# Performance work log

Hardware: AMD Instinct MI355X
Metric: run time of the kernel (lower is better)

## Reference

```python
import jax, jax.numpy as jnp
import numpy as np

DELTA_V = 0.5
DELTA_D = 3.0
ALPHA = 1.0
BETA = 1.0
GAMMA = 0.001
K = 5  # max instance label (labels 1..K; 0 = background)


def setup_inputs() -> dict:
    key = jax.random.key(0)
    k1, k2 = jax.random.split(key)
    B, D, H, W = 8, 8, 512, 1024
    embedding = jax.random.normal(k1, (B, D, H, W), dtype=jnp.float32)
    instance_mask = jax.random.randint(k2, (B, H, W), 0, K + 1, dtype=jnp.int32)
    return {"embedding": embedding, "instance_mask": instance_mask}


def _disc_loss(embedding, instance_mask):
    B, D, H, W = embedding.shape
    P = H * W
    emb = embedding.transpose(0, 2, 3, 1).reshape(B, P, D)      # [B,P,D]
    labels = instance_mask.reshape(B, P)                         # [B,P]

    # one-hot over instance labels 1..K (background excluded)
    onehot = (labels[..., None] == jnp.arange(1, K + 1, dtype=labels.dtype)).astype(emb.dtype)  # [B,P,K]
    counts = onehot.sum(axis=1)                                  # [B,K]
    present = counts > 0                                         # [B,K]
    presentf = present.astype(emb.dtype)
    N = presentf.sum(axis=-1)                                    # [B] num instances

    # per-instance centers via segment mean
    sums = jnp.einsum('bpd,bpk->bkd', emb, onehot)               # [B,K,D]
    centers = sums / jnp.maximum(counts, 1.0)[..., None]         # [B,K,D]

    # ---- variance loss: per-pixel distance to own center ----
    idx = jnp.clip(labels - 1, 0, K - 1)                         # [B,P]
    c_pix = jnp.take_along_axis(centers, idx[..., None], axis=1) # [B,P,D]
    d = jnp.sqrt(jnp.sum((emb - c_pix) ** 2, axis=-1))           # [B,P]
    val = jnp.maximum(d - DELTA_V, 0.0) ** 2                     # [B,P]
    inst_sum = jnp.einsum('bp,bpk->bk', val, onehot)             # [B,K]
    inst_mean = inst_sum / jnp.maximum(counts, 1.0)
    loss_var_b = (inst_mean * presentf).sum(-1) / jnp.maximum(N, 1.0)  # [B]

    # ---- distance loss: pairwise center hinge ----
    diff = centers[:, :, None, :] - centers[:, None, :, :]       # [B,K,K,D]
    dist_sq = jnp.sum(diff ** 2, axis=-1)                        # [B,K,K]
    iu = jnp.triu(jnp.ones((K, K), dtype=bool), k=1)             # i<j
    pair_mask = present[:, :, None] & present[:, None, :] & iu   # [B,K,K]
    safe_dist = jnp.sqrt(jnp.where(pair_mask, dist_sq, 1.0))
    term = jnp.maximum(2.0 * DELTA_D - safe_dist, 0.0) ** 2 * pair_mask.astype(emb.dtype)
    n_pairs = N * (N - 1.0) / 2.0
    loss_dist_b = term.sum((-1, -2)) / jnp.where(N > 1, n_pairs, 1.0)  # [B]

    # ---- regularization: mean norm of present centers ----
    c_norm = jnp.sqrt(jnp.where(present, jnp.sum(centers ** 2, axis=-1), 1.0))
    loss_reg_b = (c_norm * presentf).sum(-1) / jnp.maximum(N, 1.0)     # [B]

    # ---- batch mean over images that have at least one instance ----
    has = (N > 0).astype(emb.dtype)                              # [B]
    denom = jnp.maximum(has.sum(), 1.0)
    loss_var = (loss_var_b * has).sum() / denom
    loss_dist = (loss_dist_b * has).sum() / denom
    loss_reg = (loss_reg_b * has).sum() / denom
    total = ALPHA * loss_var + BETA * loss_dist + GAMMA * loss_reg
    return (total, loss_var, loss_dist, loss_reg)


def reference(embedding, instance_mask):
    return _disc_loss(embedding, instance_mask)
```

## Files before the change

### kernel.cpp

```cpp
#include <hip/hip_runtime.h>
#include <math.h>

constexpr int NB   = 8;
constexpr int ND   = 8;
constexpr int NH   = 512;
constexpr int NW   = 1024;
constexpr int NP   = NH * NW;
constexpr int NG   = NP / 4;
constexpr int BPB  = 256;
constexpr int GPB  = NG / BPB;
constexpr int NK   = 5;
constexpr int NVAL = NK * ND + NK;

constexpr float DELTA_V     = 0.5f;
constexpr float TWO_DELTA_D = 6.0f;
constexpr float GAMMA       = 0.001f;

__device__ __forceinline__ float wave_sum(float v) {
#pragma unroll
    for (int off = 32; off > 0; off >>= 1) v += __shfl_down(v, off, 64);
    return v;
}

__global__ __launch_bounds__(256) void pass1_kernel(const float* __restrict__ emb,
                                                    const int* __restrict__ mask,
                                                    float* __restrict__ sums,
                                                    float* __restrict__ cnts) {
    const int b   = blockIdx.x / BPB;
    const int blk = blockIdx.x % BPB;
    const long base = (long)blk * GPB;

    const float4* __restrict__ emb4 = (const float4*)emb + (long)b * ND * NG;
    const int4*   __restrict__ m4p  = (const int4*)mask + (long)b * NG;

    float4 zero4 = make_float4(0.f, 0.f, 0.f, 0.f);
    float4 a0l = zero4, a0h = zero4, a1l = zero4, a1h = zero4;
    float4 a2l = zero4, a2h = zero4, a3l = zero4, a3h = zero4;
    float4 a4l = zero4, a4h = zero4;
    float  n0 = 0.f, n1 = 0.f, n2 = 0.f, n3 = 0.f, n4 = 0.f;

    for (int it = threadIdx.x; it < GPB; it += 256) {
        const long g = base + it;
        const int4  m  = m4p[g];
        const float4 e0 = emb4[g];
        const float4 e1 = emb4[g + (long)NG];
        const float4 e2 = emb4[g + 2L * NG];
        const float4 e3 = emb4[g + 3L * NG];
        const float4 e4 = emb4[g + 4L * NG];
        const float4 e5 = emb4[g + 5L * NG];
        const float4 e6 = emb4[g + 6L * NG];
        const float4 e7 = emb4[g + 7L * NG];

#define KUPD1(KK, AL, AH, CN) { const float is = (lab == (KK)) ? 1.f : 0.f; CN += is; \
        AL.x = fmaf(is, f0, AL.x); AL.y = fmaf(is, f1, AL.y); \
        AL.z = fmaf(is, f2, AL.z); AL.w = fmaf(is, f3, AL.w); \
        AH.x = fmaf(is, f4, AH.x); AH.y = fmaf(is, f5, AH.y); \
        AH.z = fmaf(is, f6, AH.z); AH.w = fmaf(is, f7, AH.w); }

#define PIX1(LAB, CM) { const int lab = (LAB); \
        const float f0 = e0.CM, f1 = e1.CM, f2 = e2.CM, f3 = e3.CM; \
        const float f4 = e4.CM, f5 = e5.CM, f6 = e6.CM, f7 = e7.CM; \
        KUPD1(1, a0l, a0h, n0) KUPD1(2, a1l, a1h, n1) KUPD1(3, a2l, a2h, n2) \
        KUPD1(4, a3l, a3h, n3) KUPD1(5, a4l, a4h, n4) }

        PIX1(m.x, x) PIX1(m.y, y) PIX1(m.z, z) PIX1(m.w, w)
#undef PIX1
#undef KUPD1
    }

    __shared__ float part[4][NVAL];
    const int lane = threadIdx.x & 63;
    const int wave = threadIdx.x >> 6;
#define RED1(V, IDX) { const float r = wave_sum(V); if (lane == 0) part[wave][IDX] = r; }
#define REDK1(AL, AH, CN, K) \
    RED1(AL.x, (K)*8 + 0) RED1(AL.y, (K)*8 + 1) RED1(AL.z, (K)*8 + 2) RED1(AL.w, (K)*8 + 3) \
    RED1(AH.x, (K)*8 + 4) RED1(AH.y, (K)*8 + 5) RED1(AH.z, (K)*8 + 6) RED1(AH.w, (K)*8 + 7) \
    RED1(CN, 40 + (K))
    REDK1(a0l, a0h, n0, 0) REDK1(a1l, a1h, n1, 1) REDK1(a2l, a2h, n2, 2)
    REDK1(a3l, a3h, n3, 3) REDK1(a4l, a4h, n4, 4)
#undef REDK1
#undef RED1
    __syncthreads();
    if (threadIdx.x < NVAL) {
        const float s = part[0][threadIdx.x] + part[1][threadIdx.x] +
                        part[2][threadIdx.x] + part[3][threadIdx.x];
        if (threadIdx.x < NK * ND)
            atomicAdd(&sums[b * NK * ND + threadIdx.x], s);
        else
            atomicAdd(&cnts[b * NK + (threadIdx.x - NK * ND)], s);
    }
}

__global__ __launch_bounds__(256) void pass2_kernel(const float* __restrict__ emb,
                                                    const int* __restrict__ mask,
                                                    const float* __restrict__ sums,
                                                    const float* __restrict__ cnts,
                                                    float* __restrict__ vsums) {
    const int b   = blockIdx.x / BPB;
    const int blk = blockIdx.x % BPB;
    const long base = (long)blk * GPB;

    const float* sp = sums + b * NK * ND;
    const float inv0 = 1.f / fmaxf(cnts[b * NK + 0], 1.f);
    const float inv1 = 1.f / fmaxf(cnts[b * NK + 1], 1.f);
    const float inv2 = 1.f / fmaxf(cnts[b * NK + 2], 1.f);
    const float inv3 = 1.f / fmaxf(cnts[b * NK + 3], 1.f);
    const float inv4 = 1.f / fmaxf(cnts[b * NK + 4], 1.f);
    const float4 c0l = make_float4(sp[0]*inv0,  sp[1]*inv0,  sp[2]*inv0,  sp[3]*inv0);
    const float4 c0h = make_float4(sp[4]*inv0,  sp[5]*inv0,  sp[6]*inv0,  sp[7]*inv0);
    const float4 c1l = make_float4(sp[8]*inv1,  sp[9]*inv1,  sp[10]*inv1, sp[11]*inv1);
    const float4 c1h = make_float4(sp[12]*inv1, sp[13]*inv1, sp[14]*inv1, sp[15]*inv1);
    const float4 c2l = make_float4(sp[16]*inv2, sp[17]*inv2, sp[18]*inv2, sp[19]*inv2);
    const float4 c2h = make_float4(sp[20]*inv2, sp[21]*inv2, sp[22]*inv2, sp[23]*inv2);
    const float4 c3l = make_float4(sp[24]*inv3, sp[25]*inv3, sp[26]*inv3, sp[27]*inv3);
    const float4 c3h = make_float4(sp[28]*inv3, sp[29]*inv3, sp[30]*inv3, sp[31]*inv3);
    const float4 c4l = make_float4(sp[32]*inv4, sp[33]*inv4, sp[34]*inv4, sp[35]*inv4);
    const float4 c4h = make_float4(sp[36]*inv4, sp[37]*inv4, sp[38]*inv4, sp[39]*inv4);

    const float4* __restrict__ emb4 = (const float4*)emb + (long)b * ND * NG;
    const int4*   __restrict__ m4p  = (const int4*)mask + (long)b * NG;

    float v0 = 0.f, v1 = 0.f, v2 = 0.f, v3 = 0.f, v4 = 0.f;

    for (int it = threadIdx.x; it < GPB; it += 256) {
        const long g = base + it;
        const int4  m  = m4p[g];
        const float4 e0 = emb4[g];
        const float4 e1 = emb4[g + (long)NG];
        const float4 e2 = emb4[g + 2L * NG];
        const float4 e3 = emb4[g + 3L * NG];
        const float4 e4 = emb4[g + 4L * NG];
        const float4 e5 = emb4[g + 5L * NG];
        const float4 e6 = emb4[g + 6L * NG];
        const float4 e7 = emb4[g + 7L * NG];

#define SEL2(F) ((lab == 1) ? c0##F : (lab == 2) ? c1##F : (lab == 3) ? c2##F : \
                 (lab == 4) ? c3##F : c4##F)
#define PIX2(LAB, CM) { const int lab = (LAB); \
        const float f0 = e0.CM, f1 = e1.CM, f2 = e2.CM, f3 = e3.CM; \
        const float f4 = e4.CM, f5 = e5.CM, f6 = e6.CM, f7 = e7.CM; \
        float dd = f0 - SEL2(l.x); float dsq = dd * dd; \
        dd = f1 - SEL2(l.y); dsq = fmaf(dd, dd, dsq); \
        dd = f2 - SEL2(l.z); dsq = fmaf(dd, dd, dsq); \
        dd = f3 - SEL2(l.w); dsq = fmaf(dd, dd, dsq); \
        dd = f4 - SEL2(h.x); dsq = fmaf(dd, dd, dsq); \
        dd = f5 - SEL2(h.y); dsq = fmaf(dd, dd, dsq); \
        dd = f6 - SEL2(h.z); dsq = fmaf(dd, dd, dsq); \
        dd = f7 - SEL2(h.w); dsq = fmaf(dd, dd, dsq); \
        const float dist = sqrtf(dsq); \
        const float hv = fmaxf(dist - DELTA_V, 0.f); \
        const float val = hv * hv; \
        v0 += (lab == 1) ? val : 0.f; v1 += (lab == 2) ? val : 0.f; \
        v2 += (lab == 3) ? val : 0.f; v3 += (lab == 4) ? val : 0.f; \
        v4 += (lab == 5) ? val : 0.f; }

        PIX2(m.x, x) PIX2(m.y, y) PIX2(m.z, z) PIX2(m.w, w)
#undef PIX2
#undef SEL2
    }

    __shared__ float part[4][NK];
    const int lane = threadIdx.x & 63;
    const int wave = threadIdx.x >> 6;
#define RED2(V, IDX) { const float r = wave_sum(V); if (lane == 0) part[wave][IDX] = r; }
    RED2(v0, 0) RED2(v1, 1) RED2(v2, 2) RED2(v3, 3) RED2(v4, 4)
#undef RED2
    __syncthreads();
    if (threadIdx.x < NK) {
        const float s = part[0][threadIdx.x] + part[1][threadIdx.x] +
                        part[2][threadIdx.x] + part[3][threadIdx.x];
        atomicAdd(&vsums[b * NK + threadIdx.x], s);
    }
}

__global__ void final_kernel(const float* __restrict__ sums,
                             const float* __restrict__ cnts,
                             const float* __restrict__ vsums,
                             float* __restrict__ out) {
    __shared__ float bl[4][NB];
    const int bb = threadIdx.x;
    if (bb < NB) {
        float cc[NK];
        bool  pres[NK];
        float c[NK][ND];
        float N = 0.f;
#pragma unroll
        for (int k = 0; k < NK; ++k) {
            cc[k]   = cnts[bb * NK + k];
            pres[k] = cc[k] > 0.f;
            if (pres[k]) N += 1.f;
            const float inv = 1.f / fmaxf(cc[k], 1.f);
#pragma unroll
            for (int d = 0; d < ND; ++d)
                c[k][d] = sums[bb * NK * ND + k * ND + d] * inv;
        }
        float lv = 0.f;
#pragma unroll
        for (int k = 0; k < NK; ++k)
            if (pres[k]) lv += vsums[bb * NK + k] / fmaxf(cc[k], 1.f);
        lv /= fmaxf(N, 1.f);
        float ld = 0.f;
#pragma unroll
        for (int i = 0; i < NK; ++i)
#pragma unroll
            for (int j = i + 1; j < NK; ++j)
                if (pres[i] && pres[j]) {
                    float dsq = 0.f;
#pragma unroll
                    for (int d = 0; d < ND; ++d) {
                        const float df = c[i][d] - c[j][d];
                        dsq = fmaf(df, df, dsq);
                    }
                    const float t = fmaxf(TWO_DELTA_D - sqrtf(dsq), 0.f);
                    ld += t * t;
                }
        const float npairs = N * (N - 1.f) * 0.5f;
        ld /= (N > 1.f) ? npairs : 1.f;
        float lr = 0.f;
#pragma unroll
        for (int k = 0; k < NK; ++k)
            if (pres[k]) {
                float sq = 0.f;
#pragma unroll
                for (int d = 0; d < ND; ++d) sq = fmaf(c[k][d], c[k][d], sq);
                lr += sqrtf(sq);
            }
        lr /= fmaxf(N, 1.f);

        const float has = (N > 0.f) ? 1.f : 0.f;
        bl[0][bb] = lv * has;
        bl[1][bb] = ld * has;
        bl[2][bb] = lr * has;
        bl[3][bb] = has;
    }
    __syncthreads();
    if (threadIdx.x == 0) {
        float tv = 0.f, td = 0.f, tr = 0.f, hs = 0.f;
        for (int i = 0; i < NB; ++i) {
            tv += bl[0][i]; td += bl[1][i]; tr += bl[2][i]; hs += bl[3][i];
        }
        const float denom = fmaxf(hs, 1.f);
        tv /= denom; td /= denom; tr /= denom;
        out[0] = tv + td + GAMMA * tr;
        out[1] = tv;
        out[2] = td;
        out[3] = tr;
    }
}

extern "C" void kernel_launch(void* const* d_in, const int* in_sizes, int n_in,
                              void* d_out, int out_size, void* d_ws, size_t ws_size,
                              hipStream_t stream) {
    const float* emb  = (const float*)d_in[0];
    const int*   mask = (const int*)d_in[1];
    float* out = (float*)d_out;

    float* sums  = (float*)d_ws;
    float* cnts  = sums + NB * NK * ND;
    float* vsums = cnts + NB * NK;

    hipMemsetAsync(d_ws, 0, (size_t)(NB * NK * ND + 2 * NB * NK) * sizeof(float), stream);

    dim3 grid(NB * BPB), block(256);
    pass1_kernel<<<grid, block, 0, stream>>>(emb, mask, sums, cnts);
    pass2_kernel<<<grid, block, 0, stream>>>(emb, mask, sums, cnts, vsums);
    final_kernel<<<1, 64, 0, stream>>>(sums, cnts, vsums, out);
}
```

Measured before the change: 257.4 us.

## Split pass1 work per embedding channel and fuse the final reduction into pass2

Pass1 now gives each half-wave one embedding channel, so a thread loads one float4 plus the mask and keeps 5 accumulators instead of 40. This cuts register pressure, and the launch bound asks for higher occupancy. The mask is reloaded 8 times, once per channel, which adds cached traffic. Pass2 drops the separate final kernel by using a last-block ticket counter, and reads the centers as wave-uniform values through readfirstlane. The ticket counter adds atomics and fences at the end of every block.

```diff
diff --git a/kernel.cpp b/kernel.cpp
--- a/kernel.cpp
+++ b/kernel.cpp
@@ -7,146 +7,148 @@
 constexpr int NW   = 1024;
 constexpr int NP   = NH * NW;
 constexpr int NG   = NP / 4;
-constexpr int BPB  = 256;
-constexpr int GPB  = NG / BPB;
 constexpr int NK   = 5;
-constexpr int NVAL = NK * ND + NK;
+
+constexpr int BPB1 = 256;
+constexpr int GPB1 = NG / BPB1;
+constexpr int IT1  = GPB1 / 32;
+constexpr int BPB2 = 256;
+constexpr int GPB2 = NG / BPB2;
 
 constexpr float DELTA_V     = 0.5f;
 constexpr float TWO_DELTA_D = 6.0f;
 constexpr float GAMMA       = 0.001f;
 
+__device__ __forceinline__ float rfl(float x) {
+    return __int_as_float(__builtin_amdgcn_readfirstlane(__float_as_int(x)));
+}
+
 __device__ __forceinline__ float wave_sum(float v) {
 #pragma unroll
     for (int off = 32; off > 0; off >>= 1) v += __shfl_down(v, off, 64);
     return v;
 }
 
-__global__ __launch_bounds__(256) void pass1_kernel(const float* __restrict__ emb,
-                                                    const int* __restrict__ mask,
-                                                    float* __restrict__ sums,
-                                                    float* __restrict__ cnts) {
-    const int b   = blockIdx.x / BPB;
-    const int blk = blockIdx.x % BPB;
-    const long base = (long)blk * GPB;
+__global__ __launch_bounds__(256, 8) void pass1_kernel(const float* __restrict__ emb,
+                                                       const int* __restrict__ mask,
+                                                       float* __restrict__ sums,
+                                                       float* __restrict__ cnts) {
+    const int b    = blockIdx.x / BPB1;
+    const int blk  = blockIdx.x % BPB1;
+    const int wave = threadIdx.x >> 6;
+    const int lane = threadIdx.x & 63;
+    const int gl   = lane & 31;
+    const int d    = wave * 2 + (lane >> 5);
+    const bool dzero = (d == 0);
+
+    const float4* __restrict__ ep = (const float4*)emb + (long)(b * ND + d) * NG;
+    const int4*   __restrict__ mp = (const int4*)mask + (long)b * NG;
+
+    float a0 = 0.f, a1 = 0.f, a2 = 0.f, a3 = 0.f, a4 = 0.f;
+    float n0 = 0.f, n1 = 0.f, n2 = 0.f, n3 = 0.f, n4 = 0.f;
+
+    const int base = blk * GPB1 + gl;
+#pragma unroll 4
+    for (int it = 0; it < IT1; ++it) {
+        const int g = base + it * 32;
+        const int4   m = mp[g];
+        const float4 e = ep[g];
+#define PIX(LAB, EJ) { const int lab = (LAB); const float ej = (EJ); \
+        a0 += (lab == 1) ? ej : 0.f; a1 += (lab == 2) ? ej : 0.f; \
+        a2 += (lab == 3) ? ej : 0.f; a3 += (lab == 4) ? ej : 0.f; \
+        a4 += (lab == 5) ? ej : 0.f; \
+        if (dzero) { n0 += (lab == 1) ? 1.f : 0.f; n1 += (lab == 2) ? 1.f : 0.f; \
+                     n2 += (lab == 3) ? 1.f : 0.f; n3 += (lab == 4) ? 1.f : 0.f; \
+                     n4 += (lab == 5) ? 1.f : 0.f; } }
+        PIX(m.x, e.x) PIX(m.y, e.y) PIX(m.z, e.z) PIX(m.w, e.w)
+#undef PIX
+    }
+
+#pragma unroll
+    for (int off = 16; off > 0; off >>= 1) {
+        a0 += __shfl_down(a0, off, 32); a1 += __shfl_down(a1, off, 32);
+        a2 += __shfl_down(a2, off, 32); a3 += __shfl_down(a3, off, 32);
+        a4 += __shfl_down(a4, off, 32);
+    }
+    if (wave == 0) {
+#pragma unroll
+        for (int off = 16; off > 0; off >>= 1) {
+            n0 += __shfl_down(n0, off, 32); n1 += __shfl_down(n1, off, 32);
+            n2 += __shfl_down(n2, off, 32); n3 += __shfl_down(n3, off, 32);
+            n4 += __shfl_down(n4, off, 32);
+        }
+    }
+
+    __shared__ float pl[ND][NK];
+    __shared__ float pc[NK];
+    if (gl == 0) {
+        pl[d][0] = a0; pl[d][1] = a1; pl[d][2] = a2; pl[d][3] = a3; pl[d][4] = a4;
+    }
+    if (threadIdx.x == 0) { pc[0] = n0; pc[1] = n1; pc[2] = n2; pc[3] = n3; pc[4] = n4; }
+    __syncthreads();
+    const int t = threadIdx.x;
+    if (t < NK * ND)
+        atomicAdd(&sums[b * NK * ND + t], pl[t & 7][t >> 3]);
+    else if (t < NK * ND + NK)
+        atomicAdd(&cnts[b * NK + (t - NK * ND)], pc[t - NK * ND]);
+}
+
+__global__ __launch_bounds__(256, 6) void pass2_kernel(const float* __restrict__ emb,
+                                                       const int* __restrict__ mask,
+                                                       const float* __restrict__ sums,
+                                                       const float* __restrict__ cnts,
+                                                       float* __restrict__ vsums,
+                                                       int* __restrict__ ticket,
+                                                       float* __restrict__ out) {
+    const int b   = blockIdx.x / BPB2;
+    const int blk = blockIdx.x % BPB2;
+    const int base = blk * GPB2;
+
+    const float* sp = sums + b * NK * ND;
+    const float i0 = rfl(1.f / fmaxf(cnts[b * NK + 0], 1.f));
+    const float i1 = rfl(1.f / fmaxf(cnts[b * NK + 1], 1.f));
+    const float i2 = rfl(1.f / fmaxf(cnts[b * NK + 2], 1.f));
+    const float i3 = rfl(1.f / fmaxf(cnts[b * NK + 3], 1.f));
+    const float i4 = rfl(1.f / fmaxf(cnts[b * NK + 4], 1.f));
+    const float4 c0l = make_float4(rfl(sp[0])*i0,  rfl(sp[1])*i0,  rfl(sp[2])*i0,  rfl(sp[3])*i0);
+    const float4 c0h = make_float4(rfl(sp[4])*i0,  rfl(sp[5])*i0,  rfl(sp[6])*i0,  rfl(sp[7])*i0);
+    const float4 c1l = make_float4(rfl(sp[8])*i1,  rfl(sp[9])*i1,  rfl(sp[10])*i1, rfl(sp[11])*i1);
+    const float4 c1h = make_float4(rfl(sp[12])*i1, rfl(sp[13])*i1, rfl(sp[14])*i1, rfl(sp[15])*i1);
+    const float4 c2l = make_float4(rfl(sp[16])*i2, rfl(sp[17])*i2, rfl(sp[18])*i2, rfl(sp[19])*i2);
+    const float4 c2h = make_float4(rfl(sp[20])*i2, rfl(sp[21])*i2, rfl(sp[22])*i2, rfl(sp[23])*i2);
+    const float4 c3l = make_float4(rfl(sp[24])*i3, rfl(sp[25])*i3, rfl(sp[26])*i3, rfl(sp[27])*i3);
+    const float4 c3h = make_float4(rfl(sp[28])*i3, rfl(sp[29])*i3, rfl(sp[30])*i3, rfl(sp[31])*i3);
+    const float4 c4l = make_float4(rfl(sp[32])*i4, rfl(sp[33])*i4, rfl(sp[34])*i4, rfl(sp[35])*i4);
+    const float4 c4h = make_float4(rfl(sp[36])*i4, rfl(sp[37])*i4, rfl(sp[38])*i4, rfl(sp[39])*i4);
 
     const float4* __restrict__ emb4 = (const float4*)emb + (long)b * ND * NG;
     const int4*   __restrict__ m4p  = (const int4*)mask + (long)b * NG;
 
-    float4 zero4 = make_float4(0.f, 0.f, 0.f, 0.f);
-    float4 a0l = zero4, a0h = zero4, a1l = zero4, a1h = zero4;
-    float4 a2l = zero4, a2h = zero4, a3l = zero4, a3h = zero4;
-    float4 a4l = zero4, a4h = zero4;
-    float  n0 = 0.f, n1 = 0.f, n2 = 0.f, n3 = 0.f, n4 = 0.f;
-
-    for (int it = threadIdx.x; it < GPB; it += 256) {
-        const long g = base + it;
-        const int4  m  = m4p[g];
+    float v0 = 0.f, v1 = 0.f, v2 = 0.f, v3 = 0.f, v4 = 0.f;
+
+    for (int it = threadIdx.x; it < GPB2; it += 256) {
+        const int g = base + it;
+        const int4   m  = m4p[g];
         const float4 e0 = emb4[g];
-        const float4 e1 = emb4[g + (long)NG];
-        const float4 e2 = emb4[g + 2L * NG];
-        const float4 e3 = emb4[g + 3L * NG];
-        const float4 e4 = emb4[g + 4L * NG];
-        const float4 e5 = emb4[g + 5L * NG];
-        const float4 e6 = emb4[g + 6L * NG];
-        const float4 e7 = emb4[g + 7L * NG];
-
-#define KUPD1(KK, AL, AH, CN) { const float is = (lab == (KK)) ? 1.f : 0.f; CN += is; \
-        AL.x = fmaf(is, f0, AL.x); AL.y = fmaf(is, f1, AL.y); \
-        AL.z = fmaf(is, f2, AL.z); AL.w = fmaf(is, f3, AL.w); \
-        AH.x = fmaf(is, f4, AH.x); AH.y = fmaf(is, f5, AH.y); \
-        AH.z = fmaf(is, f6, AH.z); AH.w = fmaf(is, f7, AH.w); }
-
-#define PIX1(LAB, CM) { const int lab = (LAB); \
-        const float f0 = e0.CM, f1 = e1.CM, f2 = e2.CM, f3 = e3.CM; \
-        const float f4 = e4.CM, f5 = e5.CM, f6 = e6.CM, f7 = e7.CM; \
-        KUPD1(1, a0l, a0h, n0) KUPD1(2, a1l, a1h, n1) KUPD1(3, a2l, a2h, n2) \
-        KUPD1(4, a3l, a3h, n3) KUPD1(5, a4l, a4h, n4) }
-
-        PIX1(m.x, x) PIX1(m.y, y) PIX1(m.z, z) PIX1(m.w, w)
-#undef PIX1
-#undef KUPD1
-    }
-
-    __shared__ float part[4][NVAL];
-    const int lane = threadIdx.x & 63;
-    const int wave = threadIdx.x >> 6;
-#define RED1(V, IDX) { const float r = wave_sum(V); if (lane == 0) part[wave][IDX] = r; }
-#define REDK1(AL, AH, CN, K) \
-    RED1(AL.x, (K)*8 + 0) RED1(AL.y, (K)*8 + 1) RED1(AL.z, (K)*8 + 2) RED1(AL.w, (K)*8 + 3) \
-    RED1(AH.x, (K)*8 + 4) RED1(AH.y, (K)*8 + 5) RED1(AH.z, (K)*8 + 6) RED1(AH.w, (K)*8 + 7) \
-    RED1(CN, 40 + (K))
-    REDK1(a0l, a0h, n0, 0) REDK1(a1l, a1h, n1, 1) REDK1(a2l, a2h, n2, 2)
-    REDK1(a3l, a3h, n3, 3) REDK1(a4l, a4h, n4, 4)
-#undef REDK1
-#undef RED1
-    __syncthreads();
-    if (threadIdx.x < NVAL) {
-        const float s = part[0][threadIdx.x] + part[1][threadIdx.x] +
-                        part[2][threadIdx.x] + part[3][threadIdx.x];
-        if (threadIdx.x < NK * ND)
-            atomicAdd(&sums[b * NK * ND + threadIdx.x], s);
-        else
-            atomicAdd(&cnts[b * NK + (threadIdx.x - NK * ND)], s);
-    }
-}
-
-__global__ __launch_bounds__(256) void pass2_kernel(const float* __restrict__ emb,
-                                                    const int* __restrict__ mask,
-                                                    const float* __restrict__ sums,
-                                                    const float* __restrict__ cnts,
-                                                    float* __restrict__ vsums) {
-    const int b   = blockIdx.x / BPB;
-    const int blk = blockIdx.x % BPB;
-    const long base = (long)blk * GPB;
-
-    const float* sp = sums + b * NK * ND;
-    const float inv0 = 1.f / fmaxf(cnts[b * NK + 0], 1.f);
-    const float inv1 = 1.f / fmaxf(cnts[b * NK + 1], 1.f);
-    const float inv2 = 1.f / fmaxf(cnts[b * NK + 2], 1.f);
-    const float inv3 = 1.f / fmaxf(cnts[b * NK + 3], 1.f);
-    const float inv4 = 1.f / fmaxf(cnts[b * NK + 4], 1.f);
-    const float4 c0l = make_float4(sp[0]*inv0,  sp[1]*inv0,  sp[2]*inv0,  sp[3]*inv0);
-    const float4 c0h = make_float4(sp[4]*inv0,  sp[5]*inv0,  sp[6]*inv0,  sp[7]*inv0);
-    const float4 c1l = make_float4(sp[8]*inv1,  sp[9]*inv1,  sp[10]*inv1, sp[11]*inv1);
-    const float4 c1h = make_float4(sp[12]*inv1, sp[13]*inv1, sp[14]*inv1, sp[15]*inv1);
-    const float4 c2l = make_float4(sp[16]*inv2, sp[17]*inv2, sp[18]*inv2, sp[19]*inv2);
-    const float4 c2h = make_float4(sp[20]*inv2, sp[21]*inv2, sp[22]*inv2, sp[23]*inv2);
-    const float4 c3l = make_float4(sp[24]*inv3, sp[25]*inv3, sp[26]*inv3, sp[27]*inv3);
-    const float4 c3h = make_float4(sp[28]*inv3, sp[29]*inv3, sp[30]*inv3, sp[31]*inv3);
-    const float4 c4l = make_float4(sp[32]*inv4, sp[33]*inv4, sp[34]*inv4, sp[35]*inv4);
-    const float4 c4h = make_float4(sp[36]*inv4, sp[37]*inv4, sp[38]*inv4, sp[39]*inv4);
-
-    const float4* __restrict__ emb4 = (const float4*)emb + (long)b * ND * NG;
-    const int4*   __restrict__ m4p  = (const int4*)mask + (long)b * NG;
-
-    float v0 = 0.f, v1 = 0.f, v2 = 0.f, v3 = 0.f, v4 = 0.f;
-
-    for (int it = threadIdx.x; it < GPB; it += 256) {
-        const long g = base + it;
-        const int4  m  = m4p[g];
-        const float4 e0 = emb4[g];
-        const float4 e1 = emb4[g + (long)NG];
-        const float4 e2 = emb4[g + 2L * NG];
-        const float4 e3 = emb4[g + 3L * NG];
-        const float4 e4 = emb4[g + 4L * NG];
-        const float4 e5 = emb4[g + 5L * NG];
-        const float4 e6 = emb4[g + 6L * NG];
-        const float4 e7 = emb4[g + 7L * NG];
+        const float4 e1 = emb4[g + NG];
+        const float4 e2 = emb4[g + 2 * NG];
+        const float4 e3 = emb4[g + 3 * NG];
+        const float4 e4 = emb4[g + 4 * NG];
+        const float4 e5 = emb4[g + 5 * NG];
+        const float4 e6 = emb4[g + 6 * NG];
+        const float4 e7 = emb4[g + 7 * NG];
 
 #define SEL2(F) ((lab == 1) ? c0##F : (lab == 2) ? c1##F : (lab == 3) ? c2##F : \
                  (lab == 4) ? c3##F : c4##F)
 #define PIX2(LAB, CM) { const int lab = (LAB); \
-        const float f0 = e0.CM, f1 = e1.CM, f2 = e2.CM, f3 = e3.CM; \
-        const float f4 = e4.CM, f5 = e5.CM, f6 = e6.CM, f7 = e7.CM; \
-        float dd = f0 - SEL2(l.x); float dsq = dd * dd; \
-        dd = f1 - SEL2(l.y); dsq = fmaf(dd, dd, dsq); \
-        dd = f2 - SEL2(l.z); dsq = fmaf(dd, dd, dsq); \
-        dd = f3 - SEL2(l.w); dsq = fmaf(dd, dd, dsq); \
-        dd = f4 - SEL2(h.x); dsq = fmaf(dd, dd, dsq); \
-        dd = f5 - SEL2(h.y); dsq = fmaf(dd, dd, dsq); \
-        dd = f6 - SEL2(h.z); dsq = fmaf(dd, dd, dsq); \
-        dd = f7 - SEL2(h.w); dsq = fmaf(dd, dd, dsq); \
+        float dd = e0.CM - SEL2(l.x); float dsq = dd * dd; \
+        dd = e1.CM - SEL2(l.y); dsq = fmaf(dd, dd, dsq); \
+        dd = e2.CM - SEL2(l.z); dsq = fmaf(dd, dd, dsq); \
+        dd = e3.CM - SEL2(l.w); dsq = fmaf(dd, dd, dsq); \
+        dd = e4.CM - SEL2(h.x); dsq = fmaf(dd, dd, dsq); \
+        dd = e5.CM - SEL2(h.y); dsq = fmaf(dd, dd, dsq); \
+        dd = e6.CM - SEL2(h.z); dsq = fmaf(dd, dd, dsq); \
+        dd = e7.CM - SEL2(h.w); dsq = fmaf(dd, dd, dsq); \
         const float dist = sqrtf(dsq); \
         const float hv = fmaxf(dist - DELTA_V, 0.f); \
         const float val = hv * hv; \
@@ -171,12 +173,17 @@
                         part[2][threadIdx.x] + part[3][threadIdx.x];
         atomicAdd(&vsums[b * NK + threadIdx.x], s);
     }
-}
-
-__global__ void final_kernel(const float* __restrict__ sums,
-                             const float* __restrict__ cnts,
-                             const float* __restrict__ vsums,
-                             float* __restrict__ out) {
+    __syncthreads();
+
+    __shared__ int lastflag;
+    if (threadIdx.x == 0) {
+        __threadfence();
+        lastflag = (atomicAdd(ticket, 1) == NB * BPB2 - 1) ? 1 : 0;
+    }
+    __syncthreads();
+    if (!lastflag) return;
+    __threadfence();
+
     __shared__ float bl[4][NB];
     const int bb = threadIdx.x;
     if (bb < NB) {
@@ -191,13 +198,15 @@
             if (pres[k]) N += 1.f;
             const float inv = 1.f / fmaxf(cc[k], 1.f);
 #pragma unroll
-            for (int d = 0; d < ND; ++d)
-                c[k][d] = sums[bb * NK * ND + k * ND + d] * inv;
+            for (int dd2 = 0; dd2 < ND; ++dd2)
+                c[k][dd2] = sums[bb * NK * ND + k * ND + dd2] * inv;
         }
         float lv = 0.f;
 #pragma unroll
-        for (int k = 0; k < NK; ++k)
-            if (pres[k]) lv += vsums[bb * NK + k] / fmaxf(cc[k], 1.f);
+        for (int k = 0; k < NK; ++k) {
+            const float vs = atomicAdd(&vsums[bb * NK + k], 0.f);
+            if (pres[k]) lv += vs / fmaxf(cc[k], 1.f);
+        }
         lv /= fmaxf(N, 1.f);
         float ld = 0.f;
 #pragma unroll
@@ -207,12 +216,12 @@
                 if (pres[i] && pres[j]) {
                     float dsq = 0.f;
 #pragma unroll
-                    for (int d = 0; d < ND; ++d) {
-                        const float df = c[i][d] - c[j][d];
+                    for (int dd2 = 0; dd2 < ND; ++dd2) {
+                        const float df = c[i][dd2] - c[j][dd2];
                         dsq = fmaf(df, df, dsq);
                     }
-                    const float t = fmaxf(TWO_DELTA_D - sqrtf(dsq), 0.f);
-                    ld += t * t;
+                    const float tt = fmaxf(TWO_DELTA_D - sqrtf(dsq), 0.f);
+                    ld += tt * tt;
                 }
         const float npairs = N * (N - 1.f) * 0.5f;
         ld /= (N > 1.f) ? npairs : 1.f;
@@ -222,7 +231,7 @@
             if (pres[k]) {
                 float sq = 0.f;
 #pragma unroll
-                for (int d = 0; d < ND; ++d) sq = fmaf(c[k][d], c[k][d], sq);
+                for (int dd2 = 0; dd2 < ND; ++dd2) sq = fmaf(c[k][dd2], c[k][dd2], sq);
                 lr += sqrtf(sq);
             }
         lr /= fmaxf(N, 1.f);
@@ -255,14 +264,16 @@
     const int*   mask = (const int*)d_in[1];
     float* out = (float*)d_out;
 
-    float* sums  = (float*)d_ws;
-    float* cnts  = sums + NB * NK * ND;
-    float* vsums = cnts + NB * NK;
-
-    hipMemsetAsync(d_ws, 0, (size_t)(NB * NK * ND + 2 * NB * NK) * sizeof(float), stream);
-
-    dim3 grid(NB * BPB), block(256);
-    pass1_kernel<<<grid, block, 0, stream>>>(emb, mask, sums, cnts);
-    pass2_kernel<<<grid, block, 0, stream>>>(emb, mask, sums, cnts, vsums);
-    final_kernel<<<1, 64, 0, stream>>>(sums, cnts, vsums, out);
-}
+    float* sums   = (float*)d_ws;
+    float* cnts   = sums + NB * NK * ND;
+    float* vsums  = cnts + NB * NK;
+    int*   ticket = (int*)(vsums + NB * NK);
+
+    hipMemsetAsync(d_ws, 0,
+                   (size_t)(NB * NK * ND + 2 * NB * NK) * sizeof(float) + sizeof(int),
+                   stream);
+
+    pass1_kernel<<<dim3(NB * BPB1), dim3(256), 0, stream>>>(emb, mask, sums, cnts);
+    pass2_kernel<<<dim3(NB * BPB2), dim3(256), 0, stream>>>(emb, mask, sums, cnts,
+                                                            vsums, ticket, out);
+}
```

New measurement: 398.9 us. +55.0%, slower.
